# Kernel optimization log

Measured on AMD Instinct MI355X. Metric: run time of the kernel, lower is better.

Reference implementation:

```python
import jax, jax.numpy as jnp
import numpy as np

H, HD, S = 12, 64, 64  # num_heads, head_dim, sparse_dim (module requires head_dim == sparse_dim)
D = H * HD             # input_dim = 768 (hardcoded in original .view(-1, n, 768))
SCALE = 1.0 / float(np.sqrt(HD))


def setup_inputs() -> dict:
    key = jax.random.key(0)
    ks = jax.random.split(key, 8)
    sc = 0.02
    return {
        "x": jax.random.normal(ks[0], (8, 2048, D), jnp.float32),
        "y": jax.random.normal(ks[1], (8, 2048, D), jnp.float32),
        "Wq": jax.random.normal(ks[2], (D, D), jnp.float32) * sc,
        "bq": jnp.zeros((D,), jnp.float32),
        "Wkv": jax.random.normal(ks[3], (D, 2 * D), jnp.float32) * sc,
        "bkv": jnp.zeros((2 * D,), jnp.float32),
        "Wo": jax.random.normal(ks[4], (D, D), jnp.float32) * sc,
        "bo": jnp.zeros((D,), jnp.float32),
    }


def reference(x, y, Wq, bq, Wkv, bkv, Wo, bo):
    b, t, _ = x.shape
    _, n, _ = y.shape
    # projections (torch Linear with W stored as (in, out) here)
    q = (x @ Wq + bq).reshape(b, t, H, HD).transpose(0, 2, 1, 3)        # (b,H,t,hd)
    kv = (y @ Wkv + bkv).reshape(b, n, 2, H, HD).transpose(2, 0, 3, 1, 4)
    k, v = kv[0], kv[1]                                                 # (b,H,n,hd)
    # Original slices scores to [:S,:S] BEFORE softmax -> only that block is
    # ever used, so compute just the SxS block (same math, no full t x n matrix).
    scores = jnp.einsum('bhsd,bhzd->bhsz', q[:, :, :S], k[:, :, :S]) * SCALE
    attn = jax.nn.softmax(scores, axis=-1)                              # (b,H,S,S)
    # Original order: v @ attn (not attn @ v); valid because hd == S.
    out = jnp.einsum('bhnd,bhds->bhns', v, attn)                        # (b,H,n,S)
    out = out.transpose(0, 2, 1, 3).reshape(b, n, D)                    # (b,n,768)
    return out @ Wo + bo + y
```

## Files before the change

### kernel.cpp

```cpp
#include <hip/hip_runtime.h>
#include <hip/hip_bf16.h>

typedef __attribute__((ext_vector_type(8))) short bf16x8;
typedef __attribute__((ext_vector_type(4))) float f32x4;

#define NB 8
#define NT 2048
#define ND 768
#define NH 12
#define SCALE 0.125f
#define NKT 24

__device__ __forceinline__ ushort f2b(float f) {
  __hip_bfloat16 h = __float2bfloat16(f);
  return __builtin_bit_cast(ushort, h);
}
__device__ __forceinline__ float b2f(ushort u) {
  return __builtin_bit_cast(float, (unsigned int)u << 16);
}

#define GLDS(gp, lp)                                                        \
  __builtin_amdgcn_global_load_lds(                                         \
      (const __attribute__((address_space(1))) unsigned int*)(gp),          \
      (__attribute__((address_space(3))) unsigned int*)(lp), 16, 0, 0)

__global__ __launch_bounds__(256) void k0_all(
    const float* __restrict__ x, const float* __restrict__ y,
    const float* __restrict__ Wq, const float* __restrict__ Wkv,
    const float* __restrict__ Wo, ushort* __restrict__ Wvb,
    ushort* __restrict__ WT, ushort* __restrict__ xyb) {
  __shared__ float tile[64][65];
  int blk = blockIdx.x, tid = threadIdx.x;
  if (blk < 2304) {
    int i = blk * 256 + tid;
    int c = i / ND, e = i % ND;
    Wvb[i] = f2b(Wkv[(size_t)c * 1536 + 768 + e]);
  } else if (blk < 2736) {
    int idx = blk - 2304;
    int which = idx / 144, t = idx % 144;
    int kt = t / 12, nt = t % 12;
    #pragma unroll
    for (int p = 0; p < 16; ++p) {
      int i = p * 256 + tid;
      int r = i >> 6, c = i & 63;
      int gk = kt * 64 + r, gn = nt * 64 + c;
      float v;
      if (which == 0) v = Wq[(size_t)gk * ND + gn];
      else if (which == 1) v = Wkv[(size_t)gk * 1536 + gn];
      else v = Wo[(size_t)gk * ND + gn];
      tile[r][c] = v;
    }
    __syncthreads();
    #pragma unroll
    for (int p = 0; p < 2; ++p) {
      int i = p * 256 + tid;
      int n = i >> 3;
      int g8 = (i & 7) * 8;
      ushort u[8];
      #pragma unroll
      for (int e = 0; e < 8; ++e) u[e] = f2b(tile[g8 + e][n]);
      *(uint4*)&WT[(size_t)which * ND * ND + (size_t)(nt * 64 + n) * ND +
                   kt * 64 + g8] = *(const uint4*)u;
    }
  } else {
    int idx = blk - 2736;
    int which = idx / 192;
    int i = (idx % 192) * 256 + tid;
    int b = i / 6144, r8 = i % 6144;
    const float* src = (which ? y : x) + (size_t)b * NT * ND + (size_t)r8 * 8;
    float4 v0 = *(const float4*)src, v1 = *(const float4*)(src + 4);
    ushort u[8];
    u[0] = f2b(v0.x); u[1] = f2b(v0.y); u[2] = f2b(v0.z); u[3] = f2b(v0.w);
    u[4] = f2b(v1.x); u[5] = f2b(v1.y); u[6] = f2b(v1.z); u[7] = f2b(v1.w);
    *(uint4*)&xyb[((size_t)which * NB + b) * 64 * ND + (size_t)r8 * 8] =
        *(const uint4*)u;
  }
}

__global__ __launch_bounds__(256) void kA_fused(
    const ushort* __restrict__ xyb, const ushort* __restrict__ WT,
    const float* __restrict__ bq, const float* __restrict__ bkv,
    ushort* __restrict__ attnb) {
  int h = blockIdx.x, b = blockIdx.y;
  const ushort* Ax = xyb + (size_t)b * 64 * ND;
  const ushort* Ay = xyb + (size_t)(NB + b) * 64 * ND;
  const ushort* Bq = WT + (size_t)(h * 64) * ND;
  const ushort* Bk = WT + (size_t)ND * ND + (size_t)(h * 64) * ND;

  __shared__ ushort Sx[64 * 64], Sy[64 * 64], Sq[64 * 64], Sk[64 * 64];
  __shared__ ushort qs[64][72], ks[64][72];
  int tid = threadIdx.x, w = tid >> 6, lane = tid & 63;
  int l15 = lane & 15, l4 = lane >> 4;
  int r0 = lane >> 3;
  int g = (lane & 7) ^ r0;

  f32x4 aq[4], ak[4];
  #pragma unroll
  for (int ni = 0; ni < 4; ++ni) { aq[ni] = {0.f,0.f,0.f,0.f}; ak[ni] = {0.f,0.f,0.f,0.f}; }

  for (int t = 0; t < 12; ++t) {
    __syncthreads();
    #pragma unroll
    for (int cc = 0; cc < 2; ++cc) {
      int c = w + cc * 4;
      int row = c * 8 + r0;
      size_t off = (size_t)row * ND + t * 64 + g * 8;
      GLDS(&Ax[off], &Sx[c * 512]);
      GLDS(&Ay[off], &Sy[c * 512]);
      GLDS(&Bq[off], &Sq[c * 512]);
      GLDS(&Bk[off], &Sk[c * 512]);
    }
    __syncthreads();
    #pragma unroll
    for (int kk = 0; kk < 2; ++kk) {
      int arow = w * 16 + l15;
      int aslot = ((kk * 4 + l4) ^ (arow & 7)) * 8;
      bf16x8 afx = *(const bf16x8*)&Sx[arow * 64 + aslot];
      bf16x8 afy = *(const bf16x8*)&Sy[arow * 64 + aslot];
      #pragma unroll
      for (int ni = 0; ni < 4; ++ni) {
        int brow = ni * 16 + l15;
        int bslot = ((kk * 4 + l4) ^ (brow & 7)) * 8;
        bf16x8 bfq = *(const bf16x8*)&Sq[brow * 64 + bslot];
        bf16x8 bfk = *(const bf16x8*)&Sk[brow * 64 + bslot];
        aq[ni] = __builtin_amdgcn_mfma_f32_16x16x32_bf16(afx, bfq, aq[ni], 0, 0, 0);
        ak[ni] = __builtin_amdgcn_mfma_f32_16x16x32_bf16(afy, bfk, ak[ni], 0, 0, 0);
      }
    }
  }
  __syncthreads();
  #pragma unroll
  for (int ni = 0; ni < 4; ++ni) {
    int col = ni * 16 + l15;
    float bvq = bq[h * 64 + col];
    float bvk = bkv[h * 64 + col];
    #pragma unroll
    for (int j = 0; j < 4; ++j) {
      int row = w * 16 + l4 * 4 + j;
      qs[row][col] = f2b(aq[ni][j] + bvq);
      ks[row][col] = f2b(ak[ni][j] + bvk);
    }
  }
  __syncthreads();
  f32x4 as_[4];
  #pragma unroll
  for (int ni = 0; ni < 4; ++ni) as_[ni] = {0.f, 0.f, 0.f, 0.f};
  #pragma unroll
  for (int kk = 0; kk < 2; ++kk) {
    int arow = w * 16 + l15;
    bf16x8 af = *(const bf16x8*)&qs[arow][kk * 32 + l4 * 8];
    #pragma unroll
    for (int ni = 0; ni < 4; ++ni) {
      bf16x8 bf = *(const bf16x8*)&ks[ni * 16 + l15][kk * 32 + l4 * 8];
      as_[ni] = __builtin_amdgcn_mfma_f32_16x16x32_bf16(af, bf, as_[ni], 0, 0, 0);
    }
  }
  ushort* dst = attnb + (size_t)(b * NH + h) * 64 * 64;
  #pragma unroll
  for (int j = 0; j < 4; ++j) {
    float v[4];
    #pragma unroll
    for (int ni = 0; ni < 4; ++ni) v[ni] = as_[ni][j] * SCALE;
    float m = fmaxf(fmaxf(v[0], v[1]), fmaxf(v[2], v[3]));
    #pragma unroll
    for (int d = 1; d < 16; d <<= 1) m = fmaxf(m, __shfl_xor(m, d));
    float e[4], s = 0.f;
    #pragma unroll
    for (int ni = 0; ni < 4; ++ni) { e[ni] = expf(v[ni] - m); s += e[ni]; }
    #pragma unroll
    for (int d = 1; d < 16; d <<= 1) s += __shfl_xor(s, d);
    float rs = 1.0f / s;
    int row = w * 16 + l4 * 4 + j;
    #pragma unroll
    for (int ni = 0; ni < 4; ++ni)
      dst[row * 64 + ni * 16 + l15] = f2b(e[ni] * rs);
  }
}

__global__ __launch_bounds__(256) void k2_mfma(const ushort* __restrict__ attnb,
                                               const ushort* __restrict__ WT,
                                               ushort* __restrict__ PT) {
  int jt = blockIdx.x, h = blockIdx.y, b = blockIdx.z;
  const ushort* Ag = WT + (size_t)2 * ND * ND + (size_t)jt * 128 * ND + h * 64;
  const ushort* Bg = attnb + (size_t)(b * NH + h) * 64 * 64;

  __shared__ ushort As[128 * 64];
  __shared__ ushort Bs[64 * 64];
  int tid = threadIdx.x, w = tid >> 6, lane = tid & 63;
  int wr = (w >> 1) * 64, wc = (w & 1) * 32;
  int l15 = lane & 15, l4 = lane >> 4;
  int r0 = lane >> 3;
  int g = (lane & 7) ^ r0;

  #pragma unroll
  for (int cc = 0; cc < 4; ++cc) {
    int c = w + cc * 4;
    int row = c * 8 + r0;
    GLDS(&Ag[(size_t)row * ND + g * 8], &As[c * 512]);
  }
  #pragma unroll
  for (int cc = 0; cc < 2; ++cc) {
    int c = w + cc * 4;
    int row = c * 8 + r0;
    GLDS(&Bg[(size_t)row * 64 + g * 8], &Bs[c * 512]);
  }
  __syncthreads();

  f32x4 acc[4][2];
  #pragma unroll
  for (int mi = 0; mi < 4; ++mi)
    #pragma unroll
    for (int ni = 0; ni < 2; ++ni) acc[mi][ni] = {0.f, 0.f, 0.f, 0.f};

  #pragma unroll
  for (int kk = 0; kk < 2; ++kk) {
    bf16x8 bfr[2];
    #pragma unroll
    for (int ni = 0; ni < 2; ++ni) {
      int rb = wc + ni * 16 + l15;
      int slot = (kk * 4 + l4) ^ (rb & 7);
      bfr[ni] = *(const bf16x8*)&Bs[rb * 64 + slot * 8];
    }
    #pragma unroll
    for (int mi = 0; mi < 4; ++mi) {
      int ra = wr + mi * 16 + l15;
      int slot = (kk * 4 + l4) ^ (ra & 7);
      bf16x8 af = *(const bf16x8*)&As[ra * 64 + slot * 8];
      #pragma unroll
      for (int ni = 0; ni < 2; ++ni)
        acc[mi][ni] = __builtin_amdgcn_mfma_f32_16x16x32_bf16(af, bfr[ni],
                                                              acc[mi][ni], 0, 0, 0);
    }
  }
  #pragma unroll
  for (int mi = 0; mi < 4; ++mi)
    #pragma unroll
    for (int ni = 0; ni < 2; ++ni) {
      int d = wc + ni * 16 + l15;
      #pragma unroll
      for (int j = 0; j < 4; ++j) {
        int jr = jt * 128 + wr + mi * 16 + l4 * 4 + j;
        PT[(size_t)b * ND * ND + (size_t)jr * ND + h * 64 + d] = f2b(acc[mi][ni][j]);
      }
    }
}

__global__ __launch_bounds__(256) void k2b_f(const ushort* __restrict__ attnb,
                                             const float* __restrict__ Wo,
                                             const float* __restrict__ bkv,
                                             const float* __restrict__ bo,
                                             float* __restrict__ cvec) {
  int jt = blockIdx.x, b = blockIdx.y;
  int tid = threadIdx.x;
  __shared__ float bl[768];
  __shared__ f32x4 red[256];
  for (int i = tid; i < ND; i += 256) {
    int h = i >> 6, s = i & 63;
    const ushort* at = attnb + (size_t)(b * NH + h) * 64 * 64;
    float acc = 0.f;
    #pragma unroll 8
    for (int d = 0; d < 64; ++d) acc += bkv[768 + h * 64 + d] * b2f(at[d * 64 + s]);
    bl[i] = acc;
  }
  __syncthreads();
  int jq = tid & 31;
  int es = tid >> 5;
  int j0 = jt * 128 + jq * 4;
  f32x4 acc = {0.f, 0.f, 0.f, 0.f};
  #pragma unroll 8
  for (int e = es * 96; e < es * 96 + 96; ++e) {
    float4 w = *(const float4*)&Wo[(size_t)e * ND + j0];
    float bv = bl[e];
    acc[0] += bv * w.x; acc[1] += bv * w.y;
    acc[2] += bv * w.z; acc[3] += bv * w.w;
  }
  red[tid] = acc;
  __syncthreads();
  if (tid < 32) {
    f32x4 s = red[tid];
    #pragma unroll
    for (int k = 1; k < 8; ++k) {
      f32x4 r = red[tid + 32 * k];
      s[0] += r[0]; s[1] += r[1]; s[2] += r[2]; s[3] += r[3];
    }
    #pragma unroll
    for (int c = 0; c < 4; ++c)
      cvec[b * ND + j0 + c] = s[c] + bo[j0 + c];
  }
}

__global__ __launch_bounds__(256, 3) void k3_gemm(const ushort* __restrict__ PT,
                                                  const ushort* __restrict__ Wvb,
                                                  ushort* __restrict__ MT) {
  int flat = blockIdx.x;
  int b = flat & 7;
  int t = flat >> 3;
  int rowt = t / 6, colt = t % 6;
  const ushort* Ag = PT + (size_t)b * ND * ND + (size_t)rowt * 128 * ND;
  const ushort* Bg = Wvb + (size_t)colt * 128 * ND;
  ushort* Cout = MT + (size_t)b * ND * ND + (size_t)rowt * 128 * ND + colt * 128;

  __shared__ ushort As[2][128 * 32];
  __shared__ ushort Bs[2][128 * 32];
  int tid = threadIdx.x, w = tid >> 6, lane = tid & 63;
  int wr = (w >> 1) * 64, wc = (w & 1) * 64;
  int l15 = lane & 15, l4 = lane >> 4;
  int r0 = lane >> 2, q = lane & 3;

  f32x4 acc[4][4];
  #pragma unroll
  for (int mi = 0; mi < 4; ++mi)
    #pragma unroll
    for (int ni = 0; ni < 4; ++ni) acc[mi][ni] = {0.f, 0.f, 0.f, 0.f};

  auto STAGE = [&](int bufi, int kk) {
    #pragma unroll
    for (int cc = 0; cc < 2; ++cc) {
      int c = w + cc * 4;
      int row = c * 16 + r0;
      int sq = (q ^ ((row >> 1) & 3)) * 8;
      GLDS(&Ag[(size_t)row * ND + kk + sq], &As[bufi][c * 512]);
      GLDS(&Bg[(size_t)row * ND + kk + sq], &Bs[bufi][c * 512]);
    }
  };

  STAGE(0, 0);
  __syncthreads();
  int cur = 0;
  for (int t2 = 0; t2 < NKT; ++t2) {
    if (t2 + 1 < NKT) STAGE(cur ^ 1, (t2 + 1) * 32);
    bf16x8 af[4], bfr[4];
    #pragma unroll
    for (int mi = 0; mi < 4; ++mi) {
      int r = wr + mi * 16 + l15;
      af[mi] = *(const bf16x8*)&As[cur][r * 32 + (l4 ^ ((r >> 1) & 3)) * 8];
    }
    #pragma unroll
    for (int ni = 0; ni < 4; ++ni) {
      int r = wc + ni * 16 + l15;
      bfr[ni] = *(const bf16x8*)&Bs[cur][r * 32 + (l4 ^ ((r >> 1) & 3)) * 8];
    }
    #pragma unroll
    for (int mi = 0; mi < 4; ++mi)
      #pragma unroll
      for (int ni = 0; ni < 4; ++ni)
        acc[mi][ni] = __builtin_amdgcn_mfma_f32_16x16x32_bf16(af[mi], bfr[ni],
                                                              acc[mi][ni], 0, 0, 0);
    __syncthreads();
    cur ^= 1;
  }
  bool diagt = (rowt == colt);
  #pragma unroll
  for (int mi = 0; mi < 4; ++mi)
    #pragma unroll
    for (int ni = 0; ni < 4; ++ni)
      #pragma unroll
      for (int j = 0; j < 4; ++j) {
        int r = wr + mi * 16 + l4 * 4 + j;
        int c = wc + ni * 16 + l15;
        float v = acc[mi][ni][j] + ((diagt && r == c) ? 1.0f : 0.0f);
        Cout[(size_t)r * ND + c] = f2b(v);
      }
}

__global__ __launch_bounds__(256, 3) void k4y_gemm(const float* __restrict__ y,
                                                   const ushort* __restrict__ MT,
                                                   const float* __restrict__ cvec,
                                                   float* __restrict__ out) {
  int flat = blockIdx.x;
  int work = (flat & 7) * 96 + (flat >> 3);
  int b = work / 96;
  int rem = work % 96;
  int rowt = rem / 6;
  int colt = rem % 6;
  const float* Ag = y + (size_t)b * NT * ND + (size_t)rowt * 128 * ND;
  const ushort* Bg = MT + (size_t)b * ND * ND + (size_t)colt * 128 * ND;
  float* Out = out + (size_t)b * NT * ND;

  __shared__ ushort As[2][128 * 32];
  __shared__ ushort Bs[2][128 * 32];
  int tid = threadIdx.x, w = tid >> 6, lane = tid & 63;
  int wr = (w >> 1) * 64, wc = (w & 1) * 64;
  int l15 = lane & 15, l4 = lane >> 4;
  int r0 = lane >> 2, q = lane & 3;
  int ar = tid >> 1;
  int ag0 = (tid & 1) * 2;

  f32x4 acc[4][4];
  #pragma unroll
  for (int mi = 0; mi < 4; ++mi)
    #pragma unroll
    for (int ni = 0; ni < 4; ++ni) acc[mi][ni] = {0.f, 0.f, 0.f, 0.f};

  float4 ra[4];
  auto AISSUE = [&](int kk) {
    #pragma unroll
    for (int p = 0; p < 4; ++p)
      ra[p] = *(const float4*)&Ag[(size_t)ar * ND + kk + ag0 * 8 + p * 4];
  };
  auto AWRITE = [&](int bufi) {
    ushort u[16];
    #pragma unroll
    for (int p = 0; p < 4; ++p) {
      u[p * 4 + 0] = f2b(ra[p].x); u[p * 4 + 1] = f2b(ra[p].y);
      u[p * 4 + 2] = f2b(ra[p].z); u[p * 4 + 3] = f2b(ra[p].w);
    }
    int g0 = (ag0 + (ar >> 1)) & 3;
    int g1 = (ag0 + 1 + (ar >> 1)) & 3;
    *(uint4*)&As[bufi][ar * 32 + g0 * 8] = *(const uint4*)&u[0];
    *(uint4*)&As[bufi][ar * 32 + g1 * 8] = *(const uint4*)&u[8];
  };
  auto BSTAGE = [&](int bufi, int kk) {
    #pragma unroll
    for (int cc = 0; cc < 2; ++cc) {
      int c = w + cc * 4;
      int row = c * 16 + r0;
      int sq = (q ^ ((row >> 1) & 3)) * 8;
      GLDS(&Bg[(size_t)row * ND + kk + sq], &Bs[bufi][c * 512]);
    }
  };

  AISSUE(0);
  BSTAGE(0, 0);
  AWRITE(0);
  __syncthreads();
  int cur = 0;
  for (int t = 0; t < NKT; ++t) {
    bool more = (t + 1 < NKT);
    if (more) { AISSUE((t + 1) * 32); BSTAGE(cur ^ 1, (t + 1) * 32); }
    bf16x8 af[4], bfr[4];
    #pragma unroll
    for (int mi = 0; mi < 4; ++mi) {
      int r = wr + mi * 16 + l15;
      int gg = (l4 + (r >> 1)) & 3;
      af[mi] = *(const bf16x8*)&As[cur][r * 32 + gg * 8];
    }
    #pragma unroll
    for (int ni = 0; ni < 4; ++ni) {
      int r = wc + ni * 16 + l15;
      bfr[ni] = *(const bf16x8*)&Bs[cur][r * 32 + (l4 ^ ((r >> 1) & 3)) * 8];
    }
    #pragma unroll
    for (int mi = 0; mi < 4; ++mi)
      #pragma unroll
      for (int ni = 0; ni < 4; ++ni)
        acc[mi][ni] = __builtin_amdgcn_mfma_f32_16x16x32_bf16(af[mi], bfr[ni],
                                                              acc[mi][ni], 0, 0, 0);
    if (more) AWRITE(cur ^ 1);
    __syncthreads();
    cur ^= 1;
  }
  #pragma unroll
  for (int mi = 0; mi < 4; ++mi)
    #pragma unroll
    for (int ni = 0; ni < 4; ++ni) {
      int gc = colt * 128 + wc + ni * 16 + l15;
      float cv = cvec[b * ND + gc];
      #pragma unroll
      for (int j = 0; j < 4; ++j) {
        int gr = rowt * 128 + wr + mi * 16 + l4 * 4 + j;
        Out[(size_t)gr * ND + gc] = acc[mi][ni][j] + cv;
      }
    }
}

__global__ __launch_bounds__(256) void k0_prep(const float* __restrict__ Wkv,
                                               ushort* __restrict__ Wvb) {
  int i = blockIdx.x * 256 + threadIdx.x;
  int c = i / ND, e = i % ND;
  Wvb[i] = f2b(Wkv[(size_t)c * 1536 + 768 + e]);
}
__global__ __launch_bounds__(512) void k1a_qk(
    const float* __restrict__ x, const float* __restrict__ y,
    const float* __restrict__ Wq, const float* __restrict__ bq,
    const float* __restrict__ Wkv, const float* __restrict__ bkv,
    float* __restrict__ qk) {
  int h = blockIdx.x, b = blockIdx.y, which = blockIdx.z;
  const float* src = which ? y : x;
  __shared__ float sA[64][68];
  __shared__ float sB[64][68];
  int tid = threadIdx.x;
  int tx = tid & 15, ty = tid >> 4;
  float acc[2][4] = {{0.f,0.f,0.f,0.f},{0.f,0.f,0.f,0.f}};
  for (int kt = 0; kt < 12; ++kt) {
    __syncthreads();
    #pragma unroll
    for (int p = 0; p < 8; ++p) {
      int i = p * 512 + tid;
      int r = i >> 6, c = i & 63;
      sA[r][c] = src[(size_t)b * NT * ND + r * ND + kt * 64 + c];
      sB[r][c] = which ? Wkv[(size_t)(kt * 64 + r) * 1536 + h * 64 + c]
                       : Wq[(size_t)(kt * 64 + r) * ND + h * 64 + c];
    }
    __syncthreads();
    #pragma unroll 8
    for (int kk = 0; kk < 64; ++kk) {
      float4 bv = *(const float4*)&sB[kk][tx * 4];
      float a0 = sA[ty * 2 + 0][kk];
      float a1 = sA[ty * 2 + 1][kk];
      acc[0][0] += a0 * bv.x; acc[0][1] += a0 * bv.y;
      acc[0][2] += a0 * bv.z; acc[0][3] += a0 * bv.w;
      acc[1][0] += a1 * bv.x; acc[1][1] += a1 * bv.y;
      acc[1][2] += a1 * bv.z; acc[1][3] += a1 * bv.w;
    }
  }
  const float* bias = which ? bkv : bq;
  float* dst = qk + ((size_t)which * NB + b) * 64 * ND;
  #pragma unroll
  for (int i2 = 0; i2 < 2; ++i2)
    #pragma unroll
    for (int j = 0; j < 4; ++j)
      dst[(ty * 2 + i2) * ND + h * 64 + tx * 4 + j] =
          acc[i2][j] + bias[h * 64 + tx * 4 + j];
}
__global__ __launch_bounds__(256) void k1b_attn(const float* __restrict__ qk,
                                                float* __restrict__ attn) {
  int h = blockIdx.x, b = blockIdx.y;
  __shared__ float qs2[64][68];
  __shared__ float ks2[64][68];
  __shared__ float sc[64][68];
  __shared__ float rm[64], rs[64];
  int tid = threadIdx.x;
  #pragma unroll
  for (int p = 0; p < 16; ++p) {
    int i = p * 256 + tid;
    int r = i >> 6, c = i & 63;
    qs2[r][c] = qk[(size_t)b * 64 * ND + r * ND + h * 64 + c];
    ks2[r][c] = qk[(size_t)(NB + b) * 64 * ND + r * ND + h * 64 + c];
  }
  __syncthreads();
  int tx = tid & 15, ty = tid >> 4;
  float a[4][4] = {};
  #pragma unroll 8
  for (int kk = 0; kk < 64; ++kk) {
    float qv[4], kv[4];
    #pragma unroll
    for (int i = 0; i < 4; ++i) qv[i] = qs2[ty * 4 + i][kk];
    #pragma unroll
    for (int j = 0; j < 4; ++j) kv[j] = ks2[tx * 4 + j][kk];
    #pragma unroll
    for (int i = 0; i < 4; ++i)
      #pragma unroll
      for (int j = 0; j < 4; ++j) a[i][j] += qv[i] * kv[j];
  }
  #pragma unroll
  for (int i = 0; i < 4; ++i)
    #pragma unroll
    for (int j = 0; j < 4; ++j)
      sc[ty * 4 + i][tx * 4 + j] = a[i][j] * SCALE;
  __syncthreads();
  if (tid < 64) {
    float m = -1e30f;
    for (int z = 0; z < 64; ++z) m = fmaxf(m, sc[tid][z]);
    float s = 0.f;
    for (int z = 0; z < 64; ++z) s += expf(sc[tid][z] - m);
    rm[tid] = m;
    rs[tid] = 1.0f / s;
  }
  __syncthreads();
  #pragma unroll
  for (int p = 0; p < 16; ++p) {
    int i = p * 256 + tid;
    int r = i >> 6, c = i & 63;
    attn[((size_t)(b * NH + h) * 64 + r) * 64 + c] =
        expf(sc[r][c] - rm[r]) * rs[r];
  }
}
__global__ __launch_bounds__(256) void k2_pt(const float* __restrict__ attn,
                                             const float* __restrict__ Wo,
                                             ushort* __restrict__ PT) {
  int jt = blockIdx.x, h = blockIdx.y, b = blockIdx.z;
  __shared__ float at[64][64];
  int tid = threadIdx.x;
  #pragma unroll
  for (int p = 0; p < 16; ++p) {
    int i = p * 256 + tid;
    int d = i >> 6, s = i & 63;
    at[d][s] = attn[((size_t)(b * NH + h) * 64 + d) * 64 + s];
  }
  __syncthreads();
  int tx = tid & 31, ty = tid >> 5;
  int j0 = jt * 128 + tx * 4;
  float acc[8][4] = {};
  for (int s = 0; s < 64; ++s) {
    float4 w = *(const float4*)&Wo[(size_t)(h * 64 + s) * ND + j0];
    #pragma unroll
    for (int dd = 0; dd < 8; ++dd) {
      float av = at[ty * 8 + dd][s];
      acc[dd][0] += av * w.x; acc[dd][1] += av * w.y;
      acc[dd][2] += av * w.z; acc[dd][3] += av * w.w;
    }
  }
  #pragma unroll
  for (int jj = 0; jj < 4; ++jj) {
    ushort tmp[8];
    #pragma unroll
    for (int dd = 0; dd < 8; ++dd) tmp[dd] = f2b(acc[dd][jj]);
    *(uint4*)&PT[(size_t)b * ND * ND + (size_t)(j0 + jj) * ND + h * 64 + ty * 8] =
        *(const uint4*)tmp;
  }
}
__global__ __launch_bounds__(256) void k2b1_bva(const float* __restrict__ attn,
                                                const float* __restrict__ bkv,
                                                float* __restrict__ bvA) {
  int b = blockIdx.x;
  int tid = threadIdx.x;
  for (int i = tid; i < ND; i += 256) {
    int h = i >> 6, s = i & 63;
    const float* at = attn + (size_t)(b * NH + h) * 64 * 64;
    float acc = 0.f;
    #pragma unroll 8
    for (int d = 0; d < 64; ++d) acc += bkv[768 + h * 64 + d] * at[d * 64 + s];
    bvA[b * ND + i] = acc;
  }
}
__global__ __launch_bounds__(256) void k2b2_cvec(const float* __restrict__ bvA,
                                                 const float* __restrict__ Wo,
                                                 const float* __restrict__ bo,
                                                 float* __restrict__ cvec) {
  int jt = blockIdx.x, b = blockIdx.y;
  int tid = threadIdx.x;
  __shared__ float bl[768];
  __shared__ f32x4 red[256];
  for (int i = tid; i < ND; i += 256) bl[i] = bvA[b * ND + i];
  __syncthreads();
  int jq = tid & 31, es = tid >> 5;
  int j0 = jt * 128 + jq * 4;
  f32x4 acc = {0.f, 0.f, 0.f, 0.f};
  #pragma unroll 8
  for (int e = es * 96; e < es * 96 + 96; ++e) {
    float4 w = *(const float4*)&Wo[(size_t)e * ND + j0];
    float bv = bl[e];
    acc[0] += bv * w.x; acc[1] += bv * w.y;
    acc[2] += bv * w.z; acc[3] += bv * w.w;
  }
  red[tid] = acc;
  __syncthreads();
  if (tid < 32) {
    f32x4 s = red[tid];
    #pragma unroll
    for (int k = 1; k < 8; ++k) {
      f32x4 r = red[tid + 32 * k];
      s[0] += r[0]; s[1] += r[1]; s[2] += r[2]; s[3] += r[3];
    }
    #pragma unroll
    for (int c = 0; c < 4; ++c)
      cvec[b * ND + j0 + c] = s[c] + bo[j0 + c];
  }
}

extern "C" void kernel_launch(void* const* d_in, const int* in_sizes, int n_in,
                              void* d_out, int out_size, void* d_ws, size_t ws_size,
                              hipStream_t stream) {
  const float* x = (const float*)d_in[0];
  const float* y = (const float*)d_in[1];
  const float* Wq = (const float*)d_in[2];
  const float* bq = (const float*)d_in[3];
  const float* Wkv = (const float*)d_in[4];
  const float* bkv = (const float*)d_in[5];
  const float* Wo = (const float*)d_in[6];
  const float* bo = (const float*)d_in[7];
  float* out = (float*)d_out;
  char* ws = (char*)d_ws;

  ushort* attnb = (ushort*)(ws + 0);
  float*  cvecM = (float*)(ws + 786432);
  ushort* WvbM  = (ushort*)(ws + 811008);
  ushort* PTM   = (ushort*)(ws + 1990656);
  ushort* MTM   = (ushort*)(ws + 11427840);
  ushort* WT    = (ushort*)(ws + 20865024);
  ushort* xyb   = (ushort*)(ws + 24403968);
  bool MAIN = ws_size >= 25976832ull;

  if (MAIN) {
    k0_all<<<dim3(3120), 256, 0, stream>>>(x, y, Wq, Wkv, Wo, WvbM, WT, xyb);
    kA_fused<<<dim3(NH, NB), 256, 0, stream>>>(xyb, WT, bq, bkv, attnb);
    k2_mfma<<<dim3(6, NH, NB), 256, 0, stream>>>(attnb, WT, PTM);
    k2b_f<<<dim3(6, NB), 256, 0, stream>>>(attnb, Wo, bkv, bo, cvecM);
    k3_gemm<<<dim3(288), 256, 0, stream>>>(PTM, WvbM, MTM);
    k4y_gemm<<<dim3(768), 256, 0, stream>>>(y, MTM, cvecM, out);
    return;
  }

  float* qk    = (float*)(ws + 0);
  float* attn  = (float*)(ws + 3145728);
  float* cvec  = (float*)(ws + 4718592);
  ushort* Wvb  = (ushort*)(ws + 4743168);
  ushort* PT   = (ushort*)(ws + 5922816);
  ushort* MT   = (ushort*)(ws + 15360000);
  float* bvA   = (float*)(ws + 0);

  k0_prep<<<dim3(2304), 256, 0, stream>>>(Wkv, Wvb);
  k1a_qk<<<dim3(NH, NB, 2), 512, 0, stream>>>(x, y, Wq, bq, Wkv, bkv, qk);
  k1b_attn<<<dim3(NH, NB), 256, 0, stream>>>(qk, attn);
  k2_pt<<<dim3(6, NH, NB), 256, 0, stream>>>(attn, Wo, PT);
  k2b1_bva<<<dim3(NB), 256, 0, stream>>>(attn, bkv, bvA);
  k2b2_cvec<<<dim3(6, NB), 256, 0, stream>>>(bvA, Wo, bo, cvec);
  k3_gemm<<<dim3(288), 256, 0, stream>>>(PT, Wvb, MT);
  k4y_gemm<<<dim3(768), 256, 0, stream>>>(y, MT, cvec, out);
}
```

Before: 97.40 us.

## Load A operand directly into registers and widen K tile in final GEMM

The final y×M GEMM no longer stages the fp32 A operand (y) through shared memory. Each wave loads its own 32 rows straight from global memory into registers and converts them to bf16 MFMA fragments in registers. The K step grows from 32 to 64 with a wider swizzled B tile, halving loop iterations and barriers, and the wave layout changes to 32 rows by 128 columns. The trade is more per-thread global loads with less coalesced access, and B fragments are re-read from LDS for every MFMA pair.

```diff
diff --git a/kernel.cpp b/kernel.cpp
--- a/kernel.cpp
+++ b/kernel.cpp
@@ -9,7 +9,6 @@
 #define ND 768
 #define NH 12
 #define SCALE 0.125f
-#define NKT 24
 
 __device__ __forceinline__ ushort f2b(float f) {
   __hip_bfloat16 h = __float2bfloat16(f);
@@ -327,8 +326,8 @@
   STAGE(0, 0);
   __syncthreads();
   int cur = 0;
-  for (int t2 = 0; t2 < NKT; ++t2) {
-    if (t2 + 1 < NKT) STAGE(cur ^ 1, (t2 + 1) * 32);
+  for (int t2 = 0; t2 < 24; ++t2) {
+    if (t2 + 1 < 24) STAGE(cur ^ 1, (t2 + 1) * 32);
     bf16x8 af[4], bfr[4];
     #pragma unroll
     for (int mi = 0; mi < 4; ++mi) {
@@ -363,7 +362,7 @@
       }
 }
 
-__global__ __launch_bounds__(256, 3) void k4y_gemm(const float* __restrict__ y,
+__global__ __launch_bounds__(256, 3) void k4d_gemm(const float* __restrict__ y,
                                                    const ushort* __restrict__ MT,
                                                    const float* __restrict__ cvec,
                                                    float* __restrict__ out) {
@@ -377,88 +376,84 @@
   const ushort* Bg = MT + (size_t)b * ND * ND + (size_t)colt * 128 * ND;
   float* Out = out + (size_t)b * NT * ND;
 
-  __shared__ ushort As[2][128 * 32];
-  __shared__ ushort Bs[2][128 * 32];
+  __shared__ ushort Bs[2][128 * 64];
   int tid = threadIdx.x, w = tid >> 6, lane = tid & 63;
-  int wr = (w >> 1) * 64, wc = (w & 1) * 64;
   int l15 = lane & 15, l4 = lane >> 4;
-  int r0 = lane >> 2, q = lane & 3;
-  int ar = tid >> 1;
-  int ag0 = (tid & 1) * 2;
-
-  f32x4 acc[4][4];
-  #pragma unroll
-  for (int mi = 0; mi < 4; ++mi)
-    #pragma unroll
-    for (int ni = 0; ni < 4; ++ni) acc[mi][ni] = {0.f, 0.f, 0.f, 0.f};
-
-  float4 ra[4];
-  auto AISSUE = [&](int kk) {
-    #pragma unroll
-    for (int p = 0; p < 4; ++p)
-      ra[p] = *(const float4*)&Ag[(size_t)ar * ND + kk + ag0 * 8 + p * 4];
-  };
-  auto AWRITE = [&](int bufi) {
-    ushort u[16];
-    #pragma unroll
-    for (int p = 0; p < 4; ++p) {
-      u[p * 4 + 0] = f2b(ra[p].x); u[p * 4 + 1] = f2b(ra[p].y);
-      u[p * 4 + 2] = f2b(ra[p].z); u[p * 4 + 3] = f2b(ra[p].w);
-    }
-    int g0 = (ag0 + (ar >> 1)) & 3;
-    int g1 = (ag0 + 1 + (ar >> 1)) & 3;
-    *(uint4*)&As[bufi][ar * 32 + g0 * 8] = *(const uint4*)&u[0];
-    *(uint4*)&As[bufi][ar * 32 + g1 * 8] = *(const uint4*)&u[8];
+  int r0 = lane >> 3;
+  int g = (lane & 7) ^ r0;
+
+  const float* Ar0 = Ag + (size_t)(w * 32 + l15) * ND;
+  const float* Ar1 = Ar0 + (size_t)16 * ND;
+
+  f32x4 ap[2][2][2];
+  auto AL = [&](int kk) {
+    #pragma unroll
+    for (int wn = 0; wn < 2; ++wn) {
+      int base = kk + wn * 32 + l4 * 8;
+      ap[0][wn][0] = *(const f32x4*)&Ar0[base];
+      ap[0][wn][1] = *(const f32x4*)&Ar0[base + 4];
+      ap[1][wn][0] = *(const f32x4*)&Ar1[base];
+      ap[1][wn][1] = *(const f32x4*)&Ar1[base + 4];
+    }
   };
   auto BSTAGE = [&](int bufi, int kk) {
     #pragma unroll
-    for (int cc = 0; cc < 2; ++cc) {
+    for (int cc = 0; cc < 4; ++cc) {
       int c = w + cc * 4;
-      int row = c * 16 + r0;
-      int sq = (q ^ ((row >> 1) & 3)) * 8;
-      GLDS(&Bg[(size_t)row * ND + kk + sq], &Bs[bufi][c * 512]);
+      int row = c * 8 + r0;
+      GLDS(&Bg[(size_t)row * ND + kk + g * 8], &Bs[bufi][c * 512]);
     }
   };
 
-  AISSUE(0);
+  f32x4 acc[2][8];
+  #pragma unroll
+  for (int mi = 0; mi < 2; ++mi)
+    #pragma unroll
+    for (int ni = 0; ni < 8; ++ni) acc[mi][ni] = {0.f, 0.f, 0.f, 0.f};
+
+  AL(0);
   BSTAGE(0, 0);
-  AWRITE(0);
   __syncthreads();
   int cur = 0;
-  for (int t = 0; t < NKT; ++t) {
-    bool more = (t + 1 < NKT);
-    if (more) { AISSUE((t + 1) * 32); BSTAGE(cur ^ 1, (t + 1) * 32); }
-    bf16x8 af[4], bfr[4];
-    #pragma unroll
-    for (int mi = 0; mi < 4; ++mi) {
-      int r = wr + mi * 16 + l15;
-      int gg = (l4 + (r >> 1)) & 3;
-      af[mi] = *(const bf16x8*)&As[cur][r * 32 + gg * 8];
-    }
-    #pragma unroll
-    for (int ni = 0; ni < 4; ++ni) {
-      int r = wc + ni * 16 + l15;
-      bfr[ni] = *(const bf16x8*)&Bs[cur][r * 32 + (l4 ^ ((r >> 1) & 3)) * 8];
-    }
-    #pragma unroll
-    for (int mi = 0; mi < 4; ++mi)
-      #pragma unroll
-      for (int ni = 0; ni < 4; ++ni)
-        acc[mi][ni] = __builtin_amdgcn_mfma_f32_16x16x32_bf16(af[mi], bfr[ni],
-                                                              acc[mi][ni], 0, 0, 0);
-    if (more) AWRITE(cur ^ 1);
+  for (int t = 0; t < 12; ++t) {
+    bf16x8 af[2][2];
+    #pragma unroll
+    for (int mi = 0; mi < 2; ++mi)
+      #pragma unroll
+      for (int wn = 0; wn < 2; ++wn) {
+        ushort u[8];
+        #pragma unroll
+        for (int e = 0; e < 4; ++e) {
+          u[e] = f2b(ap[mi][wn][0][e]);
+          u[4 + e] = f2b(ap[mi][wn][1][e]);
+        }
+        af[mi][wn] = *(const bf16x8*)u;
+      }
+    if (t + 1 < 12) { AL((t + 1) * 64); BSTAGE(cur ^ 1, (t + 1) * 64); }
+    #pragma unroll
+    for (int wn = 0; wn < 2; ++wn)
+      #pragma unroll
+      for (int ni = 0; ni < 8; ++ni) {
+        int r = ni * 16 + l15;
+        int slot = ((wn * 4 + l4) ^ (r & 7)) * 8;
+        bf16x8 bfr = *(const bf16x8*)&Bs[cur][r * 64 + slot];
+        acc[0][ni] = __builtin_amdgcn_mfma_f32_16x16x32_bf16(af[0][wn], bfr,
+                                                             acc[0][ni], 0, 0, 0);
+        acc[1][ni] = __builtin_amdgcn_mfma_f32_16x16x32_bf16(af[1][wn], bfr,
+                                                             acc[1][ni], 0, 0, 0);
+      }
     __syncthreads();
     cur ^= 1;
   }
   #pragma unroll
-  for (int mi = 0; mi < 4; ++mi)
-    #pragma unroll
-    for (int ni = 0; ni < 4; ++ni) {
-      int gc = colt * 128 + wc + ni * 16 + l15;
+  for (int mi = 0; mi < 2; ++mi)
+    #pragma unroll
+    for (int ni = 0; ni < 8; ++ni) {
+      int gc = colt * 128 + ni * 16 + l15;
       float cv = cvec[b * ND + gc];
       #pragma unroll
       for (int j = 0; j < 4; ++j) {
-        int gr = rowt * 128 + wr + mi * 16 + l4 * 4 + j;
+        int gr = rowt * 128 + w * 32 + mi * 16 + l4 * 4 + j;
         Out[(size_t)gr * ND + gc] = acc[mi][ni][j] + cv;
       }
     }
@@ -678,7 +673,7 @@
     k2_mfma<<<dim3(6, NH, NB), 256, 0, stream>>>(attnb, WT, PTM);
     k2b_f<<<dim3(6, NB), 256, 0, stream>>>(attnb, Wo, bkv, bo, cvecM);
     k3_gemm<<<dim3(288), 256, 0, stream>>>(PTM, WvbM, MTM);
-    k4y_gemm<<<dim3(768), 256, 0, stream>>>(y, MTM, cvecM, out);
+    k4d_gemm<<<dim3(768), 256, 0, stream>>>(y, MTM, cvecM, out);
     return;
   }
 
@@ -697,5 +692,5 @@
   k2b1_bva<<<dim3(NB), 256, 0, stream>>>(attn, bkv, bvA);
   k2b2_cvec<<<dim3(6, NB), 256, 0, stream>>>(bvA, Wo, bo, cvec);
   k3_gemm<<<dim3(288), 256, 0, stream>>>(PT, Wvb, MT);
-  k4y_gemm<<<dim3(768), 256, 0, stream>>>(y, MT, cvec, out);
-}
+  k4d_gemm<<<dim3(768), 256, 0, stream>>>(y, MT, cvec, out);
+}
```

Result: slower. 105.6 us (+8.4%).

## Pre-convert y to bf16 and use triple-staged async GEMM for final projection

Applied to the files above, without the earlier changes.

When the workspace is large enough, the prep kernel also converts all of y to bf16, and a new final GEMM streams both operands straight into LDS with global_load_lds. It prefetches two k-tiles ahead and uses explicit vmcnt waits and barriers instead of converting fp32 rows in registers. This removes the per-tile fp32-to-bf16 conversion and register staging from the main GEMM. The cost is an extra full pass that reads y and writes a bf16 copy, and the new path only runs if the workspace meets the larger threshold.

```diff
diff --git a/kernel.cpp b/kernel.cpp
--- a/kernel.cpp
+++ b/kernel.cpp
@@ -9,7 +9,6 @@
 #define ND 768
 #define NH 12
 #define SCALE 0.125f
-#define NKT 24
 
 __device__ __forceinline__ ushort f2b(float f) {
   __hip_bfloat16 h = __float2bfloat16(f);
@@ -28,7 +27,8 @@
     const float* __restrict__ x, const float* __restrict__ y,
     const float* __restrict__ Wq, const float* __restrict__ Wkv,
     const float* __restrict__ Wo, ushort* __restrict__ Wvb,
-    ushort* __restrict__ WT, ushort* __restrict__ xyb) {
+    ushort* __restrict__ WT, ushort* __restrict__ xyb,
+    ushort* __restrict__ yb) {
   __shared__ float tile[64][65];
   int blk = blockIdx.x, tid = threadIdx.x;
   if (blk < 2304) {
@@ -62,7 +62,7 @@
       *(uint4*)&WT[(size_t)which * ND * ND + (size_t)(nt * 64 + n) * ND +
                    kt * 64 + g8] = *(const uint4*)u;
     }
-  } else {
+  } else if (blk < 3120) {
     int idx = blk - 2736;
     int which = idx / 192;
     int i = (idx % 192) * 256 + tid;
@@ -74,6 +74,14 @@
     u[4] = f2b(v1.x); u[5] = f2b(v1.y); u[6] = f2b(v1.z); u[7] = f2b(v1.w);
     *(uint4*)&xyb[((size_t)which * NB + b) * 64 * ND + (size_t)r8 * 8] =
         *(const uint4*)u;
+  } else {
+    int i = (blk - 3120) * 256 + tid;
+    const float4* src = (const float4*)y + (size_t)i * 2;
+    float4 v0 = src[0], v1 = src[1];
+    ushort u[8];
+    u[0] = f2b(v0.x); u[1] = f2b(v0.y); u[2] = f2b(v0.z); u[3] = f2b(v0.w);
+    u[4] = f2b(v1.x); u[5] = f2b(v1.y); u[6] = f2b(v1.z); u[7] = f2b(v1.w);
+    *(uint4*)&yb[(size_t)i * 8] = *(const uint4*)u;
   }
 }
 
@@ -327,8 +335,8 @@
   STAGE(0, 0);
   __syncthreads();
   int cur = 0;
-  for (int t2 = 0; t2 < NKT; ++t2) {
-    if (t2 + 1 < NKT) STAGE(cur ^ 1, (t2 + 1) * 32);
+  for (int t2 = 0; t2 < 24; ++t2) {
+    if (t2 + 1 < 24) STAGE(cur ^ 1, (t2 + 1) * 32);
     bf16x8 af[4], bfr[4];
     #pragma unroll
     for (int mi = 0; mi < 4; ++mi) {
@@ -361,6 +369,88 @@
         float v = acc[mi][ni][j] + ((diagt && r == c) ? 1.0f : 0.0f);
         Cout[(size_t)r * ND + c] = f2b(v);
       }
+}
+
+__global__ __launch_bounds__(256, 3) void k4c_gemm(const ushort* __restrict__ yb,
+                                                   const ushort* __restrict__ MT,
+                                                   const float* __restrict__ cvec,
+                                                   float* __restrict__ out) {
+  int flat = blockIdx.x;
+  int work = (flat & 7) * 96 + (flat >> 3);
+  int b = work / 96;
+  int rem = work % 96;
+  int rowt = rem / 6;
+  int colt = rem % 6;
+  const ushort* Ag = yb + (size_t)b * NT * ND + (size_t)rowt * 128 * ND;
+  const ushort* Bg = MT + (size_t)b * ND * ND + (size_t)colt * 128 * ND;
+  float* Out = out + (size_t)b * NT * ND;
+
+  __shared__ ushort As[2][128 * 32];
+  __shared__ ushort Bs[2][128 * 32];
+  int tid = threadIdx.x, w = tid >> 6, lane = tid & 63;
+  int wr = (w >> 1) * 64, wc = (w & 1) * 64;
+  int l15 = lane & 15, l4 = lane >> 4;
+  int r0 = lane >> 2, q = lane & 3;
+
+  f32x4 acc[4][4];
+  #pragma unroll
+  for (int mi = 0; mi < 4; ++mi)
+    #pragma unroll
+    for (int ni = 0; ni < 4; ++ni) acc[mi][ni] = {0.f, 0.f, 0.f, 0.f};
+
+  auto STAGE = [&](int bufi, int kt) {
+    #pragma unroll
+    for (int cc = 0; cc < 2; ++cc) {
+      int c = w + cc * 4;
+      int row = c * 16 + r0;
+      int sq = (q ^ ((row >> 1) & 3)) * 8;
+      GLDS(&Ag[(size_t)row * ND + kt * 32 + sq], &As[bufi][c * 512]);
+      GLDS(&Bg[(size_t)row * ND + kt * 32 + sq], &Bs[bufi][c * 512]);
+    }
+  };
+
+  STAGE(0, 0);
+  STAGE(1, 1);
+  for (int t = 0; t < 24; ++t) {
+    int cur = t & 1;
+    if (t == 23)
+      asm volatile("s_waitcnt vmcnt(0)\n\ts_barrier" ::: "memory");
+    else
+      asm volatile("s_waitcnt vmcnt(4)\n\ts_barrier" ::: "memory");
+    __builtin_amdgcn_sched_barrier(0);
+    bf16x8 af[4], bfr[4];
+    #pragma unroll
+    for (int mi = 0; mi < 4; ++mi) {
+      int r = wr + mi * 16 + l15;
+      af[mi] = *(const bf16x8*)&As[cur][r * 32 + (l4 ^ ((r >> 1) & 3)) * 8];
+    }
+    #pragma unroll
+    for (int ni = 0; ni < 4; ++ni) {
+      int r = wc + ni * 16 + l15;
+      bfr[ni] = *(const bf16x8*)&Bs[cur][r * 32 + (l4 ^ ((r >> 1) & 3)) * 8];
+    }
+    #pragma unroll
+    for (int mi = 0; mi < 4; ++mi)
+      #pragma unroll
+      for (int ni = 0; ni < 4; ++ni)
+        acc[mi][ni] = __builtin_amdgcn_mfma_f32_16x16x32_bf16(af[mi], bfr[ni],
+                                                              acc[mi][ni], 0, 0, 0);
+    asm volatile("s_barrier" ::: "memory");
+    __builtin_amdgcn_sched_barrier(0);
+    if (t + 2 < 24) STAGE(cur, t + 2);
+  }
+  #pragma unroll
+  for (int mi = 0; mi < 4; ++mi)
+    #pragma unroll
+    for (int ni = 0; ni < 4; ++ni) {
+      int gc = colt * 128 + wc + ni * 16 + l15;
+      float cv = cvec[b * ND + gc];
+      #pragma unroll
+      for (int j = 0; j < 4; ++j) {
+        int gr = rowt * 128 + wr + mi * 16 + l4 * 4 + j;
+        Out[(size_t)gr * ND + gc] = acc[mi][ni][j] + cv;
+      }
+    }
 }
 
 __global__ __launch_bounds__(256, 3) void k4y_gemm(const float* __restrict__ y,
@@ -425,8 +515,8 @@
   AWRITE(0);
   __syncthreads();
   int cur = 0;
-  for (int t = 0; t < NKT; ++t) {
-    bool more = (t + 1 < NKT);
+  for (int t = 0; t < 24; ++t) {
+    bool more = (t + 1 < 24);
     if (more) { AISSUE((t + 1) * 32); BSTAGE(cur ^ 1, (t + 1) * 32); }
     bf16x8 af[4], bfr[4];
     #pragma unroll
@@ -670,15 +760,21 @@
   ushort* MTM   = (ushort*)(ws + 11427840);
   ushort* WT    = (ushort*)(ws + 20865024);
   ushort* xyb   = (ushort*)(ws + 24403968);
+  ushort* yb    = (ushort*)(ws + 25976832);
   bool MAIN = ws_size >= 25976832ull;
+  bool T1   = ws_size >= 51142656ull;
 
   if (MAIN) {
-    k0_all<<<dim3(3120), 256, 0, stream>>>(x, y, Wq, Wkv, Wo, WvbM, WT, xyb);
+    k0_all<<<dim3(T1 ? 9264 : 3120), 256, 0, stream>>>(x, y, Wq, Wkv, Wo,
+                                                       WvbM, WT, xyb, yb);
     kA_fused<<<dim3(NH, NB), 256, 0, stream>>>(xyb, WT, bq, bkv, attnb);
     k2_mfma<<<dim3(6, NH, NB), 256, 0, stream>>>(attnb, WT, PTM);
     k2b_f<<<dim3(6, NB), 256, 0, stream>>>(attnb, Wo, bkv, bo, cvecM);
     k3_gemm<<<dim3(288), 256, 0, stream>>>(PTM, WvbM, MTM);
-    k4y_gemm<<<dim3(768), 256, 0, stream>>>(y, MTM, cvecM, out);
+    if (T1)
+      k4c_gemm<<<dim3(768), 256, 0, stream>>>(yb, MTM, cvecM, out);
+    else
+      k4y_gemm<<<dim3(768), 256, 0, stream>>>(y, MTM, cvecM, out);
     return;
   }
 
```

Measured after the change: 99.24 us. Within noise of the previous version (+1.9%).

## Deepen GEMM load pipeline to two tiles in flight with explicit vmcnt waits

Applied to the files above, without the earlier changes.

The two bf16 GEMM kernels now prefetch two k-tiles ahead instead of one. The plain __syncthreads is replaced by hand-placed s_waitcnt vmcnt/lgkmcnt plus s_barrier, with sched_barrier fences, so global-to-LDS loads overlap more MFMA work. The point is to hide global memory latency in the main loops. The hand-counted vmcnt values must match the number of outstanding loads exactly, and the inline asm constrains the compiler's scheduling.

```diff
diff --git a/kernel.cpp b/kernel.cpp
--- a/kernel.cpp
+++ b/kernel.cpp
@@ -9,7 +9,6 @@
 #define ND 768
 #define NH 12
 #define SCALE 0.125f
-#define NKT 24
 
 __device__ __forceinline__ ushort f2b(float f) {
   __hip_bfloat16 h = __float2bfloat16(f);
@@ -289,13 +288,13 @@
   }
 }
 
-__global__ __launch_bounds__(256, 3) void k3_gemm(const ushort* __restrict__ PT,
-                                                  const ushort* __restrict__ Wvb,
-                                                  ushort* __restrict__ MT) {
+__global__ __launch_bounds__(256, 3) void k3p_gemm(const ushort* __restrict__ PT,
+                                                   const ushort* __restrict__ Wvb,
+                                                   ushort* __restrict__ MT) {
   int flat = blockIdx.x;
   int b = flat & 7;
-  int t = flat >> 3;
-  int rowt = t / 6, colt = t % 6;
+  int t0 = flat >> 3;
+  int rowt = t0 / 6, colt = t0 % 6;
   const ushort* Ag = PT + (size_t)b * ND * ND + (size_t)rowt * 128 * ND;
   const ushort* Bg = Wvb + (size_t)colt * 128 * ND;
   ushort* Cout = MT + (size_t)b * ND * ND + (size_t)rowt * 128 * ND + colt * 128;
@@ -313,22 +312,26 @@
     #pragma unroll
     for (int ni = 0; ni < 4; ++ni) acc[mi][ni] = {0.f, 0.f, 0.f, 0.f};
 
-  auto STAGE = [&](int bufi, int kk) {
+  auto STAGE = [&](int bufi, int kt) {
     #pragma unroll
     for (int cc = 0; cc < 2; ++cc) {
       int c = w + cc * 4;
       int row = c * 16 + r0;
       int sq = (q ^ ((row >> 1) & 3)) * 8;
-      GLDS(&Ag[(size_t)row * ND + kk + sq], &As[bufi][c * 512]);
-      GLDS(&Bg[(size_t)row * ND + kk + sq], &Bs[bufi][c * 512]);
+      GLDS(&Ag[(size_t)row * ND + kt * 32 + sq], &As[bufi][c * 512]);
+      GLDS(&Bg[(size_t)row * ND + kt * 32 + sq], &Bs[bufi][c * 512]);
     }
   };
 
   STAGE(0, 0);
-  __syncthreads();
-  int cur = 0;
-  for (int t2 = 0; t2 < NKT; ++t2) {
-    if (t2 + 1 < NKT) STAGE(cur ^ 1, (t2 + 1) * 32);
+  STAGE(1, 1);
+  for (int t = 0; t < 24; ++t) {
+    int cur = t & 1;
+    if (t == 23)
+      asm volatile("s_waitcnt vmcnt(0)\n\ts_barrier" ::: "memory");
+    else
+      asm volatile("s_waitcnt vmcnt(4)\n\ts_barrier" ::: "memory");
+    __builtin_amdgcn_sched_barrier(0);
     bf16x8 af[4], bfr[4];
     #pragma unroll
     for (int mi = 0; mi < 4; ++mi) {
@@ -346,8 +349,11 @@
       for (int ni = 0; ni < 4; ++ni)
         acc[mi][ni] = __builtin_amdgcn_mfma_f32_16x16x32_bf16(af[mi], bfr[ni],
                                                               acc[mi][ni], 0, 0, 0);
-    __syncthreads();
-    cur ^= 1;
+    if (t + 2 < 24) {
+      asm volatile("s_barrier" ::: "memory");
+      __builtin_amdgcn_sched_barrier(0);
+      STAGE(cur, t + 2);
+    }
   }
   bool diagt = (rowt == colt);
   #pragma unroll
@@ -363,7 +369,7 @@
       }
 }
 
-__global__ __launch_bounds__(256, 3) void k4y_gemm(const float* __restrict__ y,
+__global__ __launch_bounds__(256, 3) void k4p_gemm(const float* __restrict__ y,
                                                    const ushort* __restrict__ MT,
                                                    const float* __restrict__ cvec,
                                                    float* __restrict__ out) {
@@ -393,10 +399,10 @@
     for (int ni = 0; ni < 4; ++ni) acc[mi][ni] = {0.f, 0.f, 0.f, 0.f};
 
   float4 ra[4];
-  auto AISSUE = [&](int kk) {
+  auto AISSUE = [&](int kt) {
     #pragma unroll
     for (int p = 0; p < 4; ++p)
-      ra[p] = *(const float4*)&Ag[(size_t)ar * ND + kk + ag0 * 8 + p * 4];
+      ra[p] = *(const float4*)&Ag[(size_t)ar * ND + kt * 32 + ag0 * 8 + p * 4];
   };
   auto AWRITE = [&](int bufi) {
     ushort u[16];
@@ -410,24 +416,28 @@
     *(uint4*)&As[bufi][ar * 32 + g0 * 8] = *(const uint4*)&u[0];
     *(uint4*)&As[bufi][ar * 32 + g1 * 8] = *(const uint4*)&u[8];
   };
-  auto BSTAGE = [&](int bufi, int kk) {
+  auto BSTAGE = [&](int bufi, int kt) {
     #pragma unroll
     for (int cc = 0; cc < 2; ++cc) {
       int c = w + cc * 4;
       int row = c * 16 + r0;
       int sq = (q ^ ((row >> 1) & 3)) * 8;
-      GLDS(&Bg[(size_t)row * ND + kk + sq], &Bs[bufi][c * 512]);
+      GLDS(&Bg[(size_t)row * ND + kt * 32 + sq], &Bs[bufi][c * 512]);
     }
   };
 
   AISSUE(0);
   BSTAGE(0, 0);
   AWRITE(0);
-  __syncthreads();
-  int cur = 0;
-  for (int t = 0; t < NKT; ++t) {
-    bool more = (t + 1 < NKT);
-    if (more) { AISSUE((t + 1) * 32); BSTAGE(cur ^ 1, (t + 1) * 32); }
+  AISSUE(1);
+  BSTAGE(1, 1);
+  for (int t = 0; t < 24; ++t) {
+    int cur = t & 1;
+    if (t == 23)
+      asm volatile("s_waitcnt vmcnt(0) lgkmcnt(0)\n\ts_barrier" ::: "memory");
+    else
+      asm volatile("s_waitcnt vmcnt(6) lgkmcnt(0)\n\ts_barrier" ::: "memory");
+    __builtin_amdgcn_sched_barrier(0);
     bf16x8 af[4], bfr[4];
     #pragma unroll
     for (int mi = 0; mi < 4; ++mi) {
@@ -446,9 +456,15 @@
       for (int ni = 0; ni < 4; ++ni)
         acc[mi][ni] = __builtin_amdgcn_mfma_f32_16x16x32_bf16(af[mi], bfr[ni],
                                                               acc[mi][ni], 0, 0, 0);
-    if (more) AWRITE(cur ^ 1);
-    __syncthreads();
-    cur ^= 1;
+    if (t + 1 < 24) {
+      AWRITE(cur ^ 1);
+      asm volatile("s_waitcnt lgkmcnt(0)\n\ts_barrier" ::: "memory");
+      __builtin_amdgcn_sched_barrier(0);
+      if (t + 2 < 24) {
+        AISSUE(t + 2);
+        BSTAGE(cur, t + 2);
+      }
+    }
   }
   #pragma unroll
   for (int mi = 0; mi < 4; ++mi)
@@ -677,8 +693,8 @@
     kA_fused<<<dim3(NH, NB), 256, 0, stream>>>(xyb, WT, bq, bkv, attnb);
     k2_mfma<<<dim3(6, NH, NB), 256, 0, stream>>>(attnb, WT, PTM);
     k2b_f<<<dim3(6, NB), 256, 0, stream>>>(attnb, Wo, bkv, bo, cvecM);
-    k3_gemm<<<dim3(288), 256, 0, stream>>>(PTM, WvbM, MTM);
-    k4y_gemm<<<dim3(768), 256, 0, stream>>>(y, MTM, cvecM, out);
+    k3p_gemm<<<dim3(288), 256, 0, stream>>>(PTM, WvbM, MTM);
+    k4p_gemm<<<dim3(768), 256, 0, stream>>>(y, MTM, cvecM, out);
     return;
   }
 
@@ -696,6 +712,6 @@
   k2_pt<<<dim3(6, NH, NB), 256, 0, stream>>>(attn, Wo, PT);
   k2b1_bva<<<dim3(NB), 256, 0, stream>>>(attn, bkv, bvA);
   k2b2_cvec<<<dim3(6, NB), 256, 0, stream>>>(bvA, Wo, bo, cvec);
-  k3_gemm<<<dim3(288), 256, 0, stream>>>(PT, Wvb, MT);
-  k4y_gemm<<<dim3(768), 256, 0, stream>>>(y, MT, cvec, out);
-}
+  k3p_gemm<<<dim3(288), 256, 0, stream>>>(PT, Wvb, MT);
+  k4p_gemm<<<dim3(768), 256, 0, stream>>>(y, MT, cvec, out);
+}
```

After: 102.5 us. 1.05x slower.
